# Performance work log

Measured on AMD Instinct MI355X. Metric: run time of the kernel, lower is better.

Reference implementation:

```python
import jax, jax.numpy as jnp
import numpy as np

N_OBJS = 100          # max detections / scatter buffer size
TOP_K = 100           # top_k_n peaks per channel
KP_THRES = 0.3        # score threshold before NMS
NMS_IOU = 0.5
RESIZE_H, RESIZE_W = 1536.0, 1536.0   # resize_shape (== heatmap HxW here)
H, W = 1536, 1536


def _peak_hms(hms):
    # 3x3 stride-1 SAME max pool; keep only local maxima (Base.apply_max_pool)
    hmax = jax.lax.reduce_window(hms, -jnp.inf, jax.lax.max, (1, 3, 3, 1), (1, 1, 1, 1), 'SAME')
    return jnp.where(hms == hmax, hms, 0.0)


def _top_k_loc(hms, k):
    # per-channel top-k peak coordinates -> [b, c, k, 2] (y, x) int32
    b, h, w, c = hms.shape
    flat = jnp.transpose(hms, (0, 3, 1, 2)).reshape(b, c, h * w)
    _, idx = jax.lax.top_k(flat, k)
    return jnp.stack([idx // w, idx % w], axis=-1).astype(jnp.int32)


def _iou_matrix(boxes):
    # boxes [N,4] = (y1,x1,y2,x2)
    y1, x1, y2, x2 = boxes[:, 0], boxes[:, 1], boxes[:, 2], boxes[:, 3]
    area = jnp.maximum(y2 - y1, 0.0) * jnp.maximum(x2 - x1, 0.0)
    iy1 = jnp.maximum(y1[:, None], y1[None, :]); ix1 = jnp.maximum(x1[:, None], x1[None, :])
    iy2 = jnp.minimum(y2[:, None], y2[None, :]); ix2 = jnp.minimum(x2[:, None], x2[None, :])
    inter = jnp.maximum(iy2 - iy1, 0.0) * jnp.maximum(ix2 - ix1, 0.0)
    union = area[:, None] + area[None, :] - inter
    return inter / jnp.maximum(union, 1e-8)


def _nms_single(boxes, scores):
    # greedy single-class NMS, fixed-size (combined_non_max_suppression equivalent,
    # clip_boxes=False, score_threshold=-inf); padded slots are zeros like TF.
    order = jnp.argsort(-scores)
    boxes, scores = boxes[order], scores[order]
    n = boxes.shape[0]
    iou = _iou_matrix(boxes)
    idxs = jnp.arange(n)

    def step(suppressed, inp):
        i, iou_row = inp
        keep_i = ~suppressed[i]
        return suppressed | (keep_i & (iou_row > NMS_IOU) & (idxs > i)), keep_i

    _, keep = jax.lax.scan(step, jnp.zeros(n, bool), (idxs, iou))
    perm = jnp.argsort(jnp.where(keep, 0, 1))  # stable: compact kept to front, score order preserved
    keep_s = keep[perm]
    out_boxes = jnp.where(keep_s[:, None], boxes[perm], 0.0)
    out_scores = jnp.where(keep_s, scores[perm], 0.0)
    return out_boxes, out_scores, jnp.zeros(n, jnp.float32)


def _forward(obj_heat_map, offset_map, size_maps, origin_shapes):
    resize_shape = jnp.array([RESIZE_H, RESIZE_W], jnp.float32)
    ratio = origin_shapes / resize_shape                      # [b,2]
    hms = _peak_hms(obj_heat_map)                             # [b,H,W,2]
    b = hms.shape[0]
    coors = _top_k_loc(hms, TOP_K)                            # [b,2,K,2]
    b_coors, b_lnmks = coors[:, :1], coors[:, 1:]             # obj / nose coords
    bidx = jnp.arange(b)[:, None, None]

    # nose landmark: scores at nose-channel peaks, masked mean of coords (int mean like TF)
    nose_scores = hms[bidx, b_lnmks[..., 0], b_lnmks[..., 1], 1]     # [b,1,K]
    nose_mask = nose_scores > 0.5
    cnt = jnp.maximum(jnp.sum(nose_mask), 1)
    lnmk_mean = jnp.sum(jnp.where(nose_mask[..., None], b_lnmks, 0), axis=(0, 1, 2)) // cnt
    b_lnmks_m = lnmk_mean.reshape(b, 1, 2)                    # requires b == 1 (as in original)
    b_nose_scores = jnp.where(nose_mask, nose_scores, -1.0).reshape(b, -1)

    # boxes from sizes at object peaks
    size_vals = size_maps[bidx, b_coors[..., 0], b_coors[..., 1]]    # [b,1,K,2]
    obj_scores = hms[bidx, b_coors[..., 0], b_coors[..., 1], 0]      # [b,1,K]
    centers = b_coors.astype(jnp.float32)
    tls = jnp.maximum(centers - size_vals / 2.0, 0.0)
    brs = jnp.minimum(centers + size_vals / 2.0, resize_shape - 1.0)
    bboxes = jnp.concatenate([tls, brs], axis=-1) * jnp.tile(ratio, (1, 2))[:, None, None, :]
    bboxes, scores = bboxes[:, 0], obj_scores[:, 0]           # [b,K,4], [b,K]

    # scatter masked candidates into -1-initialized buffer (tensor_scatter_nd_update equivalent)
    mask = scores > KP_THRES
    cand = jnp.where(mask[..., None], jnp.concatenate([bboxes, scores[..., None]], -1), -1.0)
    cand = jnp.pad(cand, ((0, 0), (0, N_OBJS - TOP_K), (0, 0)), constant_values=-1.0)  # [b,N_OBJS,5]

    nb, ns, nc = jax.vmap(_nms_single)(cand[..., :4], cand[..., 4])
    box_results = jnp.where(nb == -1.0, jnp.inf, nb)
    box_results = jnp.where(box_results == 0.0, jnp.inf, box_results)  # (x - 1 == -1)
    b_bboxes = jnp.concatenate([box_results, ns[..., None], nc[..., None]], axis=-1)  # [b,N_OBJS,6]

    # offset vectors at the mean nose landmark (gather 8ch -> [b,n,4,2])
    bidx2 = jnp.arange(b)[:, None]
    off = offset_map[bidx2, b_lnmks_m[..., 0], b_lnmks_m[..., 1]].reshape(b, 1, 4, 2)
    lf = b_lnmks_m.astype(jnp.float32)
    b_ENM = (lf[:, :, None, :] - off) * ratio[:, None, None, :]
    b_lnmks_out = lf * ratio[:, None, :]
    return b_bboxes, b_lnmks_out, b_ENM, b_nose_scores


def setup_inputs() -> dict:
    key = jax.random.key(0)
    k1, k2, k3 = jax.random.split(key, 3)
    obj_heat_map = jax.random.uniform(k1, (1, H, W, 2), jnp.float32)
    offset_map = jax.random.normal(k2, (1, H, W, 8), jnp.float32) * 8.0
    size_maps = jax.random.uniform(k3, (1, H, W, 2), jnp.float32) * 128.0
    origin_shapes = jnp.array([[1080.0, 1920.0]], jnp.float32)
    return {"obj_heat_map": obj_heat_map, "offset_map": offset_map,
            "size_maps": size_maps, "origin_shapes": origin_shapes}


def reference(obj_heat_map, offset_map, size_maps, origin_shapes):
    return _forward(obj_heat_map, offset_map, size_maps, origin_shapes)
```

## Files before the change

### kernel.cpp

```cpp
#include <hip/hip_runtime.h>
#include <cstdint>

#define IW 1536
#define IH 1536
#define TOPK 100
#define CAPP 327680
#define CAPB 128
#define CAPT 8192
#define BF_INF16 0x7F7Fu

typedef unsigned u32; typedef unsigned long long u64; typedef unsigned short u16;

#define OH1   0
#define OH2   512
#define OSEL  1024
#define OCNT  1032
#define OLB   1040
#define OLT   1552
#define OPK   17936

__device__ __forceinline__ u32 enc16(u32 b){ b &= 0xFFFFu; return (b & 0x8000u) ? ((~b)&0xFFFFu) : (b|0x8000u); }
__device__ __forceinline__ u32 dec16(u32 e){ return (e & 0x8000u) ? (e^0x8000u) : ((~e)&0xFFFFu); }
__device__ __forceinline__ float up16(u32 b){ return __uint_as_float((b&0xFFFFu)<<16); }
__device__ __forceinline__ u16 f2bf(float f){ u32 u=__float_as_uint(f); return (u16)((u + 0x7FFFu + ((u>>16)&1u))>>16); }

__global__ __launch_bounds__(1024) void scan_kernel(const u32* __restrict__ hm, u32* __restrict__ ws){
  __shared__ u32 lh[512];
  __shared__ u32 lbuf[2][1600];
  __shared__ u32 lcnt[2], lbase[2];
  int tid = threadIdx.x, lane = tid & 63;
  for(int i=tid;i<512;i+=1024) lh[i]=0u;
  if(tid<2) lcnt[tid]=0u;
  __syncthreads();

  int p = (blockIdx.x*1024 + tid)*4;
  int y = p / IW, x = p - y*IW;
  const u32* R1 = hm + y*IW;
  const u32* R0 = y ? R1 - IW : R1;
  const u32* R2 = (y < IH-1) ? R1 + IW : R1;
  uint4 c0 = *(const uint4*)(R0+x), c1 = *(const uint4*)(R1+x), c2 = *(const uint4*)(R2+x);
  int xl = x ? x-1 : 0, xr = (x+4 < IW) ? x+4 : IW-1;
  u32 a0[6] = {R0[xl], c0.x, c0.y, c0.z, c0.w, R0[xr]};
  u32 a1[6] = {R1[xl], c1.x, c1.y, c1.z, c1.w, R1[xr]};
  u32 a2[6] = {R2[xl], c2.x, c2.y, c2.z, c2.w, R2[xr]};

  #pragma unroll
  for(int j=0;j<4;++j){
    u32 c = a1[j+1];
    u32 cl = c & 0xFFFFu, chv = c >> 16;
    u32 m0=0u, m1=0u;
    #pragma unroll
    for(int d=0;d<3;++d){
      u32 n0=a0[j+d], n2=a2[j+d];
      u32 t;
      t=n0&0xFFFFu; m0=t>m0?t:m0;  t=n0>>16; m1=t>m1?t:m1;
      t=n2&0xFFFFu; m0=t>m0?t:m0;  t=n2>>16; m1=t>m1?t:m1;
    }
    { u32 n=a1[j]; u32 t=n&0xFFFFu; m0=t>m0?t:m0; t=n>>16; m1=t>m1?t:m1; }
    { u32 n=a1[j+2]; u32 t=n&0xFFFFu; m0=t>m0?t:m0; t=n>>16; m1=t>m1?t:m1; }
    bool p0 = (cl >= m0), p1 = (chv >= m1);

    u64 mk0 = __ballot(p0);
    if(mk0){
      u32 cntw = __popcll(mk0), b;
      if(lane==0) b = atomicAdd(&lcnt[0], cntw);
      b = __shfl(b, 0);
      if(p0){
        u32 pos = b + __popcll(mk0 & ((1ull<<lane)-1ull));
        if(pos < 1600) lbuf[0][pos] = (u32)(p+j);
      }
    }
    u64 mk1 = __ballot(p1);
    if(mk1){
      u32 cntw = __popcll(mk1), b;
      if(lane==0) b = atomicAdd(&lcnt[1], cntw);
      b = __shfl(b, 0);
      if(p1){
        u32 pos = b + __popcll(mk1 & ((1ull<<lane)-1ull));
        if(pos < 1600) lbuf[1][pos] = (u32)(p+j);
      }
    }
    if(p0) atomicAdd(&lh[enc16(cl)>>8], 1u);
    if(p1) atomicAdd(&lh[256 + (enc16(chv)>>8)], 1u);
  }
  __syncthreads();
  if(tid < 2){
    u32 n = lcnt[tid]; if(n > 1600) n = 1600;
    lcnt[tid] = n;
    lbase[tid] = atomicAdd(&ws[OCNT+tid], n);
  }
  __syncthreads();
  for(int ch=0;ch<2;++ch){
    u32 n = lcnt[ch], base = lbase[ch];
    for(u32 i=tid;i<n;i+=1024){
      u32 g = base + i;
      if(g < CAPP) ws[OPK + ch*CAPP + g] = lbuf[ch][i];
    }
  }
  for(int i=tid;i<512;i+=1024) if(lh[i]) atomicAdd(&ws[OH1+i], lh[i]);
}

__global__ void sel_msd_kernel(u32* __restrict__ ws){
  __shared__ u32 h[512];
  int t = threadIdx.x;
  h[t] = ws[OH1+t];
  __syncthreads();
  if(t < 2){
    const u32* hh = h + t*256;
    u32 above = 0; int D = 0;
    for(int b=255;b>=1;--b){
      if(above + hh[b] >= (u32)TOPK){ D = b; break; }
      above += hh[b];
    }
    ws[OSEL+t] = (u32)D;
    ws[OSEL+2+t] = above;
  }
}

__global__ __launch_bounds__(1024) void lsd_kernel(const u32* __restrict__ hm, u32* __restrict__ ws){
  __shared__ u32 lh[512];
  int tid = threadIdx.x;
  for(int i=tid;i<512;i+=1024) lh[i]=0u;
  __syncthreads();
  int D0 = (int)ws[OSEL], D1 = (int)ws[OSEL+1];
  for(int ch=0;ch<2;++ch){
    u32 n = ws[OCNT+ch]; if(n > CAPP) n = CAPP;
    int D = ch ? D1 : D0;
    for(u32 i = blockIdx.x*1024 + tid; i < n; i += gridDim.x*1024){
      u32 idx = ws[OPK + ch*CAPP + i];
      u32 e = enc16(hm[idx] >> (16*ch));
      if((int)(e>>8) == D) atomicAdd(&lh[ch*256 + (e&255)], 1u);
    }
  }
  __syncthreads();
  for(int i=tid;i<512;i+=1024) if(lh[i]) atomicAdd(&ws[OH2+i], lh[i]);
}

__global__ void sel_lsd_kernel(u32* __restrict__ ws){
  __shared__ u32 h[512];
  int t = threadIdx.x;
  h[t] = ws[OH2+t];
  __syncthreads();
  if(t < 2){
    int D = (int)ws[OSEL+t];
    int need2 = TOPK - (int)ws[OSEL+2+t];
    const u32* hh = h + t*256;
    u32 above = 0; int L = 0;
    for(int b=255;b>=1;--b){
      if((int)(above + hh[b]) >= need2){ L = b; break; }
      above += hh[b];
    }
    ws[OSEL+4+t] = (u32)((D<<8) | L);
  }
}

__global__ __launch_bounds__(1024) void collect_kernel(const u32* __restrict__ hm, u32* __restrict__ ws){
  __shared__ u32 tbuf[2][2048];
  __shared__ u32 tcnt[2], tbase[2];
  int tid = threadIdx.x, lane = tid & 63;
  if(tid<2) tcnt[tid]=0u;
  __syncthreads();
  u32 thr0 = ws[OSEL+4], thr1 = ws[OSEL+5];
  u64* listB = (u64*)(ws + OLB);
  u32 total = gridDim.x*1024;
  for(int ch=0;ch<2;++ch){
    u32 n = ws[OCNT+ch]; if(n > CAPP) n = CAPP;
    u32 thr = ch ? thr1 : thr0;
    for(u32 base = blockIdx.x*1024; base < n; base += total){
      u32 i = base + tid;
      bool act = (i < n);
      u32 idx = 0, e = 0;
      if(act){ idx = ws[OPK + ch*CAPP + i]; e = enc16(hm[idx] >> (16*ch)); }
      if(act && e > thr){
        u32 pos = atomicAdd(&ws[OCNT+2+ch], 1u);
        if(pos < CAPB) listB[ch*CAPB + pos] = ((u64)e<<32) | (u32)(~idx);
      }
      bool isT = act && (e == thr);
      u64 mk = __ballot(isT);
      if(mk){
        u32 cntw = __popcll(mk), b;
        if(lane==0) b = atomicAdd(&tcnt[ch], cntw);
        b = __shfl(b, 0);
        if(isT){
          u32 pos = b + __popcll(mk & ((1ull<<lane)-1ull));
          if(pos < 2048) tbuf[ch][pos] = idx;
        }
      }
    }
  }
  __syncthreads();
  if(tid < 2){
    u32 c = tcnt[tid]; if(c > 2048) c = 2048;
    tcnt[tid] = c;
    tbase[tid] = atomicAdd(&ws[OCNT+4+tid], c);
  }
  __syncthreads();
  for(int ch=0;ch<2;++ch)
    for(u32 i=tid;i<tcnt[ch];i+=1024){
      u32 g = tbase[ch] + i;
      if(g < CAPT) ws[OLT + ch*CAPT + g] = tbuf[ch][i];
    }
}

__global__ __launch_bounds__(1024) void finalize_kernel(
    u32* __restrict__ ws, const u32* __restrict__ szm, const u16* __restrict__ offm,
    const u16* __restrict__ orig, u16* __restrict__ out){
  __shared__ u32 cnts[8];
  __shared__ u64 keysL[CAPB];
  __shared__ u32 h2[2048];
  __shared__ u32 wbits[64];
  __shared__ u32 sel[CAPB];
  __shared__ int Bv, cntBelowS, selc;
  __shared__ float oval[TOPK]; __shared__ int oidx[TOPK];
  __shared__ float nval[TOPK]; __shared__ int nidx[TOPK];
  __shared__ float cbox[TOPK][4]; __shared__ float cscore[TOPK]; __shared__ float area[TOPK];
  __shared__ int sup[TOPK]; __shared__ int slotv[TOPK];
  __shared__ u64 nbits[2*TOPK];
  __shared__ u64 suppS[2];
  __shared__ int cS, srS, scS, meanr, meanc;
  int tid = threadIdx.x, lane = tid & 63;
  const u64* listB = (const u64*)(ws + OLB);

  if(tid < 6) cnts[tid] = ws[OCNT+tid];
  if(tid < 2) cnts[6+tid] = ws[OSEL+4+tid];
  if(tid < TOPK){ oval[tid]=0.0f; oidx[tid]=0; nval[tid]=0.0f; nidx[tid]=0; }
  __syncthreads();

  for(int ch=0; ch<2; ++ch){
    int nB = (int)cnts[2+ch]; if(nB > CAPB) nB = CAPB; if(nB > TOPK) nB = TOPK;
    u32 thr = cnts[6+ch];
    float tval = up16(dec16(thr));
    float* dval = ch ? nval : oval;
    int*   didx = ch ? nidx : oidx;

    u64 kreg = 0;
    if(tid < nB){ kreg = listB[ch*CAPB + tid]; keysL[tid] = kreg; }
    for(int i=tid;i<2048;i+=1024) h2[i]=0u;
    if(tid < 64) wbits[tid]=0u;
    if(tid == 0){ selc = 0; Bv = 0; cntBelowS = 0; }
    __syncthreads();
    if(tid < nB){
      int r = 0;
      for(int j=0;j<nB;++j) r += (keysL[j] > kreg);
      dval[r] = up16(dec16((u32)(kreg>>32)));
      didx[r] = (int)(~(u32)(kreg & 0xFFFFFFFFu));
    }
    int need = TOPK - nB;

    if(need > 0){
      int nT = (int)cnts[4+ch]; if(nT > CAPT) nT = CAPT;
      const u32* seg = ws + OLT + ch*CAPT;
      for(int i=tid;i<nT;i+=1024) atomicAdd(&h2[seg[i]>>11], 1u);
      __syncthreads();
      if(tid < 64){
        int base = tid*32;
        u32 s = 0;
        #pragma unroll
        for(int k2=0;k2<32;++k2) s += h2[base+k2];
        u32 c = s;
        #pragma unroll
        for(int off=1;off<64;off<<=1){
          u32 v = __shfl_up(c, off, 64);
          if(lane >= off) c += v;
        }
        u64 m = __ballot(c >= (u32)need);
        int L = (int)(__ffsll((unsigned long long)m) - 1);
        if(tid == L){
          u32 cum2 = c - s;
          int B = base;
          for(int k2=0;k2<32;++k2){
            u32 hb = h2[base+k2];
            if(cum2 + hb >= (u32)need){ B = base+k2; break; }
            cum2 += hb;
          }
          Bv = B; cntBelowS = (int)cum2;
        }
      }
      __syncthreads();
      int B = Bv;
      for(int i=tid;i<nT;i+=1024){
        u32 idx = seg[i];
        int b = (int)(idx>>11);
        if(b < B){
          int pos = atomicAdd(&selc, 1);
          if(pos < CAPB) sel[pos] = idx;
        } else if(b == B){
          atomicOr(&wbits[(idx&2047)>>5], 1u<<(idx&31));
        }
      }
      __syncthreads();
      int sc = selc; if(sc > CAPB) sc = CAPB;
      if(tid < sc){
        u32 v = sel[tid];
        int r = 0;
        for(int j=0;j<sc;++j) r += (sel[j] < v);
        if(nB + r < TOPK){ dval[nB+r] = tval; didx[nB+r] = (int)v; }
      }
      if(tid == 0){
        int rem = need - sc;
        int pos = nB + sc;
        for(int wi=0; wi<64 && rem>0; ++wi){
          u32 bits = wbits[wi];
          while(bits && rem>0){
            int l = __ffs(bits) - 1;
            bits &= bits - 1;
            if(pos < TOPK){ dval[pos] = tval; didx[pos] = (int)(((u32)B<<11) | ((u32)wi<<5) | (u32)l); }
            ++pos; --rem;
          }
        }
      }
    }
    __syncthreads();
  }

  float ry = up16(orig[0]) / 1536.0f;
  float rx = up16(orig[1]) / 1536.0f;

  if(tid == 0){ cS = 0; srS = 0; scS = 0; }
  __syncthreads();
  if(tid < TOPK && nval[tid] > 0.5f){
    atomicAdd(&cS, 1);
    atomicAdd(&srS, nidx[tid] / IW);
    atomicAdd(&scS, nidx[tid] % IW);
  }
  if(tid < TOPK) out[610 + tid] = f2bf(nval[tid] > 0.5f ? nval[tid] : -1.0f);
  __syncthreads();
  if(tid == 0){
    int c = cS < 1 ? 1 : cS;
    meanr = srS / c; meanc = scS / c;
  }

  if(tid < TOPK){
    int idx = oidx[tid];
    int r = idx / IW, c = idx - r*IW;
    float score = oval[tid];
    u32 sz = szm[idx];
    float sy = up16(sz), sx = up16(sz>>16);
    float cy = (float)r, cx = (float)c;
    float tly = fmaxf(cy - sy*0.5f, 0.0f);
    float tlx = fmaxf(cx - sx*0.5f, 0.0f);
    float bry = fminf(cy + sy*0.5f, 1535.0f);
    float brx = fminf(cx + sx*0.5f, 1535.0f);
    bool mk = score > 0.3f;
    float b0 = mk ? tly*ry : -1.0f;
    float b1 = mk ? tlx*rx : -1.0f;
    float b2 = mk ? bry*ry : -1.0f;
    float b3 = mk ? brx*rx : -1.0f;
    cbox[tid][0]=b0; cbox[tid][1]=b1; cbox[tid][2]=b2; cbox[tid][3]=b3;
    cscore[tid] = mk ? score : -1.0f;
    area[tid] = fmaxf(b2-b0,0.0f) * fmaxf(b3-b1,0.0f);
  }
  if(tid < 2*TOPK) nbits[tid] = 0ull;
  __syncthreads();

  for(int t=tid; t<TOPK*TOPK; t+=1024){
    int i = t / TOPK, j = t - i*TOPK;
    if(j > i){
      float iy1 = fmaxf(cbox[i][0], cbox[j][0]);
      float ix1 = fmaxf(cbox[i][1], cbox[j][1]);
      float iy2 = fminf(cbox[i][2], cbox[j][2]);
      float ix2 = fminf(cbox[i][3], cbox[j][3]);
      float inter = fmaxf(iy2-iy1,0.0f) * fmaxf(ix2-ix1,0.0f);
      float uni = (area[i] + area[j]) - inter;
      if(inter / fmaxf(uni, 1e-8f) > 0.5f)
        atomicOr(&nbits[i*2 + (j>>6)], 1ull << (j&63));
    }
  }
  __syncthreads();
  if(tid == 0){
    u64 s0 = 0ull, s1 = 0ull;
    for(int i=0;i<TOPK;++i){
      bool su = (i<64) ? ((s0>>i)&1ull) : ((s1>>(i-64))&1ull);
      if(!su){ s0 |= nbits[i*2]; s1 |= nbits[i*2+1]; }
    }
    suppS[0] = s0; suppS[1] = s1;
  }
  __syncthreads();
  if(tid < TOPK) sup[tid] = (int)((suppS[tid>>6] >> (tid&63)) & 1ull);
  __syncthreads();

  if(tid < TOPK){
    int kbefore = 0, sbefore = 0, ktot = 0;
    for(int j=0;j<TOPK;++j){
      int sj = sup[j];
      ktot += (1 - sj);
      if(j < tid){ kbefore += (1 - sj); sbefore += sj; }
    }
    int slot = sup[tid] ? (ktot + sbefore) : kbefore;
    slotv[slot] = tid;
  }
  __syncthreads();

  if(tid < TOPK){
    int s = slotv[tid];
    bool ks = !sup[s];
    u16 row[6];
    if(ks){
      for(int d=0;d<4;++d){
        float v = cbox[s][d];
        row[d] = (v == -1.0f || v == 0.0f) ? (u16)BF_INF16 : f2bf(v);
      }
      row[4] = f2bf(cscore[s]);
    } else {
      for(int d=0;d<4;++d) row[d] = (u16)BF_INF16;
      row[4] = 0;
    }
    row[5] = 0;
    for(int d=0;d<6;++d) out[tid*6 + d] = row[d];
  }

  if(tid == 0){
    float lfy = (float)meanr, lfx = (float)meanc;
    out[600] = f2bf(lfy * ry);
    out[601] = f2bf(lfx * rx);
    const u16* op = offm + ((size_t)meanr*IW + meanc)*8;
    for(int p=0;p<4;++p){
      out[602 + p*2 + 0] = f2bf((lfy - up16(op[p*2+0])) * ry);
      out[602 + p*2 + 1] = f2bf((lfx - up16(op[p*2+1])) * rx);
    }
  }
}

extern "C" void kernel_launch(void* const* d_in, const int* in_sizes, int n_in,
                              void* d_out, int out_size, void* d_ws, size_t ws_size,
                              hipStream_t stream) {
  const u32* heat = (const u32*)d_in[0];
  const u16* offm = (const u16*)d_in[1];
  const u32* szm  = (const u32*)d_in[2];
  const u16* orig = (const u16*)d_in[3];
  u16* out = (u16*)d_out;
  u32* ws = (u32*)d_ws;

  hipMemsetAsync(ws, 0, 1040*sizeof(u32), stream);
  scan_kernel<<<576, 1024, 0, stream>>>(heat, ws);
  sel_msd_kernel<<<1, 512, 0, stream>>>(ws);
  lsd_kernel<<<128, 1024, 0, stream>>>(heat, ws);
  sel_lsd_kernel<<<1, 512, 0, stream>>>(ws);
  collect_kernel<<<128, 1024, 0, stream>>>(heat, ws);
  finalize_kernel<<<1, 1024, 0, stream>>>(ws, szm, offm, orig, out);
}
```

Before: 195.9 us.

## Fuse radix-select passes into one mid kernel and store peak values compactly

The scan kernel now also writes each peak's 16-bit value alongside its index, so later passes read a compact value array instead of gathering from the heatmap. The MSD selection, LSD histogram, LSD selection and collect kernels are replaced by one mid kernel. Each block of that kernel redundantly computes the top-bin threshold with a wave-level prefix scan, then emits every candidate in or above the threshold bucket. The finalize kernel now does the low-digit histogram and tie handling itself over that candidate list. This cuts four launches and the scattered heatmap gathers, in exchange for more serial work in the single-block finalize and extra workspace traffic.

```diff
diff --git a/kernel.cpp b/kernel.cpp
--- a/kernel.cpp
+++ b/kernel.cpp
@@ -6,27 +6,51 @@
 #define TOPK 100
 #define CAPP 327680
 #define CAPB 128
-#define CAPT 8192
+#define CAPM 16384
 #define BF_INF16 0x7F7Fu
 
 typedef unsigned u32; typedef unsigned long long u64; typedef unsigned short u16;
 
 #define OH1   0
-#define OH2   512
-#define OSEL  1024
-#define OCNT  1032
-#define OLB   1040
-#define OLT   1552
-#define OPK   17936
+#define OCNT  512
+#define OSEL  516
+#define OPK   520
+#define OPV   (OPK + 2*CAPP)
+#define OMID  (OPV + CAPP)
 
 __device__ __forceinline__ u32 enc16(u32 b){ b &= 0xFFFFu; return (b & 0x8000u) ? ((~b)&0xFFFFu) : (b|0x8000u); }
 __device__ __forceinline__ u32 dec16(u32 e){ return (e & 0x8000u) ? (e^0x8000u) : ((~e)&0xFFFFu); }
 __device__ __forceinline__ float up16(u32 b){ return __uint_as_float((b&0xFFFFu)<<16); }
 __device__ __forceinline__ u16 f2bf(float f){ u32 u=__float_as_uint(f); return (u16)((u + 0x7FFFu + ((u>>16)&1u))>>16); }
 
+__device__ __forceinline__ void wave_sel256(const u32* bins, u32 need, int* Dout, u32* Aout){
+  int lane = threadIdx.x & 63;
+  u32 s = bins[lane*4] + bins[lane*4+1] + bins[lane*4+2] + bins[lane*4+3];
+  u32 c = s;
+  #pragma unroll
+  for(int off=1;off<64;off<<=1){
+    u32 v = __shfl_down(c, off, 64);
+    if(lane + off < 64) c += v;
+  }
+  u32 cnext = __shfl_down(c, 1, 64); if(lane==63) cnext = 0u;
+  u64 m = __ballot(c >= need);
+  if(m == 0ull){ if(lane==0){ *Dout = 0; *Aout = 0u; } return; }
+  int L = 63 - __builtin_clzll(m);
+  if(lane == L){
+    u32 above = cnext; int D = 4*L;
+    for(int b=4*L+3; b>=4*L; --b){
+      u32 h = bins[b];
+      if(above + h >= need){ D = b; break; }
+      above += h;
+    }
+    *Dout = D; *Aout = above;
+  }
+}
+
 __global__ __launch_bounds__(1024) void scan_kernel(const u32* __restrict__ hm, u32* __restrict__ ws){
   __shared__ u32 lh[512];
   __shared__ u32 lbuf[2][1600];
+  __shared__ u16 vbuf[2][1600];
   __shared__ u32 lcnt[2], lbase[2];
   int tid = threadIdx.x, lane = tid & 63;
   for(int i=tid;i<512;i+=1024) lh[i]=0u;
@@ -46,42 +70,42 @@
 
   #pragma unroll
   for(int j=0;j<4;++j){
-    u32 c = a1[j+1];
-    u32 cl = c & 0xFFFFu, chv = c >> 16;
+    u32 cc = a1[j+1];
+    u32 cl = cc & 0xFFFFu, chv = cc >> 16;
     u32 m0=0u, m1=0u;
     #pragma unroll
     for(int d=0;d<3;++d){
-      u32 n0=a0[j+d], n2=a2[j+d];
-      u32 t;
+      u32 n0=a0[j+d], n2=a2[j+d]; u32 t;
       t=n0&0xFFFFu; m0=t>m0?t:m0;  t=n0>>16; m1=t>m1?t:m1;
       t=n2&0xFFFFu; m0=t>m0?t:m0;  t=n2>>16; m1=t>m1?t:m1;
     }
-    { u32 n=a1[j]; u32 t=n&0xFFFFu; m0=t>m0?t:m0; t=n>>16; m1=t>m1?t:m1; }
+    { u32 n=a1[j];   u32 t=n&0xFFFFu; m0=t>m0?t:m0; t=n>>16; m1=t>m1?t:m1; }
     { u32 n=a1[j+2]; u32 t=n&0xFFFFu; m0=t>m0?t:m0; t=n>>16; m1=t>m1?t:m1; }
-    bool p0 = (cl >= m0), p1 = (chv >= m1);
-
-    u64 mk0 = __ballot(p0);
+    bool pk0 = (cl >= m0), pk1 = (chv >= m1);
+    u32 idx = (u32)(p + j);
+
+    u64 mk0 = __ballot(pk0);
     if(mk0){
-      u32 cntw = __popcll(mk0), b;
-      if(lane==0) b = atomicAdd(&lcnt[0], cntw);
+      u32 cw = __popcll(mk0), b;
+      if(lane==0) b = atomicAdd(&lcnt[0], cw);
       b = __shfl(b, 0);
-      if(p0){
+      if(pk0){
         u32 pos = b + __popcll(mk0 & ((1ull<<lane)-1ull));
-        if(pos < 1600) lbuf[0][pos] = (u32)(p+j);
-      }
-    }
-    u64 mk1 = __ballot(p1);
+        if(pos < 1600){ lbuf[0][pos] = idx; vbuf[0][pos] = (u16)cl; }
+      }
+    }
+    u64 mk1 = __ballot(pk1);
     if(mk1){
-      u32 cntw = __popcll(mk1), b;
-      if(lane==0) b = atomicAdd(&lcnt[1], cntw);
+      u32 cw = __popcll(mk1), b;
+      if(lane==0) b = atomicAdd(&lcnt[1], cw);
       b = __shfl(b, 0);
-      if(p1){
+      if(pk1){
         u32 pos = b + __popcll(mk1 & ((1ull<<lane)-1ull));
-        if(pos < 1600) lbuf[1][pos] = (u32)(p+j);
-      }
-    }
-    if(p0) atomicAdd(&lh[enc16(cl)>>8], 1u);
-    if(p1) atomicAdd(&lh[256 + (enc16(chv)>>8)], 1u);
+        if(pos < 1600){ lbuf[1][pos] = idx; vbuf[1][pos] = (u16)chv; }
+      }
+    }
+    if(pk0) atomicAdd(&lh[enc16(cl)>>8], 1u);
+    if(pk1) atomicAdd(&lh[256 + (enc16(chv)>>8)], 1u);
   }
   __syncthreads();
   if(tid < 2){
@@ -90,127 +114,80 @@
     lbase[tid] = atomicAdd(&ws[OCNT+tid], n);
   }
   __syncthreads();
+  u16* pv = (u16*)(ws + OPV);
   for(int ch=0;ch<2;++ch){
     u32 n = lcnt[ch], base = lbase[ch];
     for(u32 i=tid;i<n;i+=1024){
       u32 g = base + i;
-      if(g < CAPP) ws[OPK + ch*CAPP + g] = lbuf[ch][i];
+      if(g < CAPP){ ws[OPK + ch*CAPP + g] = lbuf[ch][i]; pv[ch*CAPP + g] = vbuf[ch][i]; }
     }
   }
   for(int i=tid;i<512;i+=1024) if(lh[i]) atomicAdd(&ws[OH1+i], lh[i]);
 }
 
-__global__ void sel_msd_kernel(u32* __restrict__ ws){
-  __shared__ u32 h[512];
-  int t = threadIdx.x;
-  h[t] = ws[OH1+t];
-  __syncthreads();
-  if(t < 2){
-    const u32* hh = h + t*256;
-    u32 above = 0; int D = 0;
-    for(int b=255;b>=1;--b){
-      if(above + hh[b] >= (u32)TOPK){ D = b; break; }
-      above += hh[b];
-    }
-    ws[OSEL+t] = (u32)D;
-    ws[OSEL+2+t] = above;
-  }
-}
-
-__global__ __launch_bounds__(1024) void lsd_kernel(const u32* __restrict__ hm, u32* __restrict__ ws){
-  __shared__ u32 lh[512];
-  int tid = threadIdx.x;
-  for(int i=tid;i<512;i+=1024) lh[i]=0u;
-  __syncthreads();
-  int D0 = (int)ws[OSEL], D1 = (int)ws[OSEL+1];
+#define GRID2 128
+__global__ __launch_bounds__(1024) void mid_kernel(u32* __restrict__ ws){
+  __shared__ u32 lhh[512];
+  __shared__ u64 mbuf[2][2048];
+  __shared__ u32 mcnt[2], mbase[2];
+  __shared__ int Dsh[2]; __shared__ u32 Ash[2];
+  int tid = threadIdx.x, lane = tid & 63;
+  if(tid < 512) lhh[tid] = ws[OH1+tid];
+  if(tid < 2) mcnt[tid] = 0u;
+  __syncthreads();
+  if(tid < 64){
+    wave_sel256(lhh,       (u32)TOPK, &Dsh[0], &Ash[0]);
+    wave_sel256(lhh + 256, (u32)TOPK, &Dsh[1], &Ash[1]);
+  }
+  __syncthreads();
+  if(blockIdx.x == 0 && tid < 2){ ws[OSEL+tid] = (u32)Dsh[tid]; ws[OSEL+2+tid] = Ash[tid]; }
+
+  const u16* pv = (const u16*)(ws + OPV);
   for(int ch=0;ch<2;++ch){
     u32 n = ws[OCNT+ch]; if(n > CAPP) n = CAPP;
-    int D = ch ? D1 : D0;
-    for(u32 i = blockIdx.x*1024 + tid; i < n; i += gridDim.x*1024){
-      u32 idx = ws[OPK + ch*CAPP + i];
-      u32 e = enc16(hm[idx] >> (16*ch));
-      if((int)(e>>8) == D) atomicAdd(&lh[ch*256 + (e&255)], 1u);
-    }
-  }
-  __syncthreads();
-  for(int i=tid;i<512;i+=1024) if(lh[i]) atomicAdd(&ws[OH2+i], lh[i]);
-}
-
-__global__ void sel_lsd_kernel(u32* __restrict__ ws){
-  __shared__ u32 h[512];
-  int t = threadIdx.x;
-  h[t] = ws[OH2+t];
-  __syncthreads();
-  if(t < 2){
-    int D = (int)ws[OSEL+t];
-    int need2 = TOPK - (int)ws[OSEL+2+t];
-    const u32* hh = h + t*256;
-    u32 above = 0; int L = 0;
-    for(int b=255;b>=1;--b){
-      if((int)(above + hh[b]) >= need2){ L = b; break; }
-      above += hh[b];
-    }
-    ws[OSEL+4+t] = (u32)((D<<8) | L);
-  }
-}
-
-__global__ __launch_bounds__(1024) void collect_kernel(const u32* __restrict__ hm, u32* __restrict__ ws){
-  __shared__ u32 tbuf[2][2048];
-  __shared__ u32 tcnt[2], tbase[2];
-  int tid = threadIdx.x, lane = tid & 63;
-  if(tid<2) tcnt[tid]=0u;
-  __syncthreads();
-  u32 thr0 = ws[OSEL+4], thr1 = ws[OSEL+5];
-  u64* listB = (u64*)(ws + OLB);
-  u32 total = gridDim.x*1024;
-  for(int ch=0;ch<2;++ch){
-    u32 n = ws[OCNT+ch]; if(n > CAPP) n = CAPP;
-    u32 thr = ch ? thr1 : thr0;
-    for(u32 base = blockIdx.x*1024; base < n; base += total){
+    int D = Dsh[ch];
+    for(u32 base = blockIdx.x*1024; base < n; base += GRID2*1024){
       u32 i = base + tid;
       bool act = (i < n);
-      u32 idx = 0, e = 0;
-      if(act){ idx = ws[OPK + ch*CAPP + i]; e = enc16(hm[idx] >> (16*ch)); }
-      if(act && e > thr){
-        u32 pos = atomicAdd(&ws[OCNT+2+ch], 1u);
-        if(pos < CAPB) listB[ch*CAPB + pos] = ((u64)e<<32) | (u32)(~idx);
-      }
-      bool isT = act && (e == thr);
-      u64 mk = __ballot(isT);
+      u32 e = 0, idx = 0;
+      if(act){ e = enc16(pv[ch*CAPP + i]); idx = ws[OPK + ch*CAPP + i]; }
+      bool hit = act && ((int)(e>>8) >= D);
+      u64 mk = __ballot(hit);
       if(mk){
-        u32 cntw = __popcll(mk), b;
-        if(lane==0) b = atomicAdd(&tcnt[ch], cntw);
+        u32 cw = __popcll(mk), b;
+        if(lane==0) b = atomicAdd(&mcnt[ch], cw);
         b = __shfl(b, 0);
-        if(isT){
+        if(hit){
           u32 pos = b + __popcll(mk & ((1ull<<lane)-1ull));
-          if(pos < 2048) tbuf[ch][pos] = idx;
+          if(pos < 2048) mbuf[ch][pos] = ((u64)e<<32) | (u32)(~idx);
         }
       }
     }
   }
   __syncthreads();
   if(tid < 2){
-    u32 c = tcnt[tid]; if(c > 2048) c = 2048;
-    tcnt[tid] = c;
-    tbase[tid] = atomicAdd(&ws[OCNT+4+tid], c);
-  }
-  __syncthreads();
+    u32 c = mcnt[tid]; if(c > 2048) c = 2048;
+    mcnt[tid] = c;
+    mbase[tid] = atomicAdd(&ws[OCNT+2+tid], c);
+  }
+  __syncthreads();
+  u64* mid = (u64*)(ws + OMID);
   for(int ch=0;ch<2;++ch)
-    for(u32 i=tid;i<tcnt[ch];i+=1024){
-      u32 g = tbase[ch] + i;
-      if(g < CAPT) ws[OLT + ch*CAPT + g] = tbuf[ch][i];
+    for(u32 i=tid;i<mcnt[ch];i+=1024){
+      u32 g = mbase[ch] + i;
+      if(g < CAPM) mid[ch*CAPM + g] = mbuf[ch][i];
     }
 }
 
 __global__ __launch_bounds__(1024) void finalize_kernel(
     u32* __restrict__ ws, const u32* __restrict__ szm, const u16* __restrict__ offm,
     const u16* __restrict__ orig, u16* __restrict__ out){
-  __shared__ u32 cnts[8];
-  __shared__ u64 keysL[CAPB];
+  __shared__ u64 keys[CAPB];
+  __shared__ u32 lsd[256];
   __shared__ u32 h2[2048];
   __shared__ u32 wbits[64];
   __shared__ u32 sel[CAPB];
-  __shared__ int Bv, cntBelowS, selc;
+  __shared__ int Bv, selc, selc2, Lsh; __shared__ u32 Aul;
   __shared__ float oval[TOPK]; __shared__ int oidx[TOPK];
   __shared__ float nval[TOPK]; __shared__ int nidx[TOPK];
   __shared__ float cbox[TOPK][4]; __shared__ float cscore[TOPK]; __shared__ float area[TOPK];
@@ -219,39 +196,59 @@
   __shared__ u64 suppS[2];
   __shared__ int cS, srS, scS, meanr, meanc;
   int tid = threadIdx.x, lane = tid & 63;
-  const u64* listB = (const u64*)(ws + OLB);
-
-  if(tid < 6) cnts[tid] = ws[OCNT+tid];
-  if(tid < 2) cnts[6+tid] = ws[OSEL+4+tid];
+
   if(tid < TOPK){ oval[tid]=0.0f; oidx[tid]=0; nval[tid]=0.0f; nidx[tid]=0; }
   __syncthreads();
 
   for(int ch=0; ch<2; ++ch){
-    int nB = (int)cnts[2+ch]; if(nB > CAPB) nB = CAPB; if(nB > TOPK) nB = TOPK;
-    u32 thr = cnts[6+ch];
-    float tval = up16(dec16(thr));
+    int nM = (int)ws[OCNT+2+ch]; if(nM > CAPM) nM = CAPM;
+    int D = (int)ws[OSEL+ch];
+    u32 above = ws[OSEL+2+ch];
+    const u64* mid = ((const u64*)(ws + OMID)) + ch*CAPM;
     float* dval = ch ? nval : oval;
     int*   didx = ch ? nidx : oidx;
 
-    u64 kreg = 0;
-    if(tid < nB){ kreg = listB[ch*CAPB + tid]; keysL[tid] = kreg; }
     for(int i=tid;i<2048;i+=1024) h2[i]=0u;
+    if(tid < 256) lsd[tid]=0u;
     if(tid < 64) wbits[tid]=0u;
-    if(tid == 0){ selc = 0; Bv = 0; cntBelowS = 0; }
+    if(tid == 0){ selc = 0; selc2 = 0; Bv = 0; }
     __syncthreads();
-    if(tid < nB){
+
+    for(int i=tid;i<nM;i+=1024){
+      u64 k = mid[i]; u32 e = (u32)(k>>32);
+      if((int)(e>>8) == D) atomicAdd(&lsd[e&255], 1u);
+      else { int pos = atomicAdd(&selc, 1); if(pos < CAPB) keys[pos] = k; }
+    }
+    __syncthreads();
+    u32 need2 = (u32)TOPK - above;
+    if(tid < 64) wave_sel256(lsd, need2, &Lsh, &Aul);
+    __syncthreads();
+    u32 thr = ((u32)D<<8) | (u32)Lsh;
+    float tval = up16(dec16(thr));
+
+    for(int i=tid;i<nM;i+=1024){
+      u64 k = mid[i]; u32 e = (u32)(k>>32);
+      if(e > thr && (e>>8) == (u32)D){
+        int pos = atomicAdd(&selc, 1); if(pos < CAPB) keys[pos] = k;
+      } else if(e == thr){
+        u32 idx = ~(u32)(k & 0xFFFFFFFFu);
+        atomicAdd(&h2[idx>>11], 1u);
+      }
+    }
+    __syncthreads();
+    int nA = selc; if(nA > CAPB) nA = CAPB; if(nA > TOPK) nA = TOPK;
+    if(tid < nA){
+      u64 kreg = keys[tid];
       int r = 0;
-      for(int j=0;j<nB;++j) r += (keysL[j] > kreg);
-      dval[r] = up16(dec16((u32)(kreg>>32)));
-      didx[r] = (int)(~(u32)(kreg & 0xFFFFFFFFu));
-    }
-    int need = TOPK - nB;
+      for(int j=0;j<nA;++j) r += (keys[j] > kreg);
+      if(r < TOPK){
+        dval[r] = up16(dec16((u32)(kreg>>32)));
+        didx[r] = (int)(~(u32)(kreg & 0xFFFFFFFFu));
+      }
+    }
+    int need = TOPK - nA;
 
     if(need > 0){
-      int nT = (int)cnts[4+ch]; if(nT > CAPT) nT = CAPT;
-      const u32* seg = ws + OLT + ch*CAPT;
-      for(int i=tid;i<nT;i+=1024) atomicAdd(&h2[seg[i]>>11], 1u);
-      __syncthreads();
       if(tid < 64){
         int base = tid*32;
         u32 s = 0;
@@ -273,32 +270,35 @@
             if(cum2 + hb >= (u32)need){ B = base+k2; break; }
             cum2 += hb;
           }
-          Bv = B; cntBelowS = (int)cum2;
+          Bv = B;
         }
       }
       __syncthreads();
       int B = Bv;
-      for(int i=tid;i<nT;i+=1024){
-        u32 idx = seg[i];
-        int b = (int)(idx>>11);
-        if(b < B){
-          int pos = atomicAdd(&selc, 1);
-          if(pos < CAPB) sel[pos] = idx;
-        } else if(b == B){
-          atomicOr(&wbits[(idx&2047)>>5], 1u<<(idx&31));
+      for(int i=tid;i<nM;i+=1024){
+        u64 k = mid[i]; u32 e = (u32)(k>>32);
+        if(e == thr){
+          u32 idx = ~(u32)(k & 0xFFFFFFFFu);
+          int b = (int)(idx>>11);
+          if(b < B){
+            int pos = atomicAdd(&selc2, 1);
+            if(pos < CAPB) sel[pos] = idx;
+          } else if(b == B){
+            atomicOr(&wbits[(idx&2047)>>5], 1u<<(idx&31));
+          }
         }
       }
       __syncthreads();
-      int sc = selc; if(sc > CAPB) sc = CAPB;
+      int sc = selc2; if(sc > CAPB) sc = CAPB;
       if(tid < sc){
         u32 v = sel[tid];
         int r = 0;
         for(int j=0;j<sc;++j) r += (sel[j] < v);
-        if(nB + r < TOPK){ dval[nB+r] = tval; didx[nB+r] = (int)v; }
+        if(nA + r < TOPK){ dval[nA+r] = tval; didx[nA+r] = (int)v; }
       }
       if(tid == 0){
         int rem = need - sc;
-        int pos = nB + sc;
+        int pos = nA + sc;
         for(int wi=0; wi<64 && rem>0; ++wi){
           u32 bits = wbits[wi];
           while(bits && rem>0){
@@ -431,11 +431,8 @@
   u16* out = (u16*)d_out;
   u32* ws = (u32*)d_ws;
 
-  hipMemsetAsync(ws, 0, 1040*sizeof(u32), stream);
+  hipMemsetAsync(ws, 0, 520*sizeof(u32), stream);
   scan_kernel<<<576, 1024, 0, stream>>>(heat, ws);
-  sel_msd_kernel<<<1, 512, 0, stream>>>(ws);
-  lsd_kernel<<<128, 1024, 0, stream>>>(heat, ws);
-  sel_lsd_kernel<<<1, 512, 0, stream>>>(ws);
-  collect_kernel<<<128, 1024, 0, stream>>>(heat, ws);
+  mid_kernel<<<GRID2, 1024, 0, stream>>>(ws);
   finalize_kernel<<<1, 1024, 0, stream>>>(ws, szm, offm, orig, out);
 }
```

Result: faster. 187.0 us (-4.6%).
